# Kernel tuning notes

Measured on AMD Instinct MI355X. Metric: run time of the kernel, lower is better.

The kernel has to match this reference:

```python
import jax, jax.numpy as jnp
import numpy as np

B = 32768
T = 1024  # num_time_bins


def setup_inputs() -> dict:
    key = jax.random.key(0)
    k1, k2, k3, k4 = jax.random.split(key, 4)
    hazard_values = jax.random.uniform(k1, (B, T), dtype=jnp.float32)
    labels_Y = jax.random.uniform(k2, (B,), dtype=jnp.float32) * T
    # nn.Linear(T, T): weight [T, T] (out, in), bias [T]
    lim = 1.0 / np.sqrt(T)
    W = jax.random.uniform(k3, (T, T), minval=-lim, maxval=lim, dtype=jnp.float32)
    b = jax.random.uniform(k4, (T,), minval=-lim, maxval=lim, dtype=jnp.float32)
    return {"hazard_values": hazard_values, "labels_Y": labels_Y, "W": W, "b": b}


def reference(hazard_values, labels_Y, W, b):
    # linear + sigmoid + argmax -> per-row truncation position
    logits = hazard_values @ W.T + b                       # [B, T]
    trunc_pos = jnp.argmax(jax.nn.sigmoid(logits), axis=1, keepdims=True)  # [B, 1] int
    # survival curve
    S = jnp.cumprod(1.0 - hazard_values, axis=1)           # [B, T]
    # vectorized truncation decay: for t >= p, multiply by exp(-(t - p))
    t = jnp.arange(T)[None, :]                             # [1, T]
    decay = jnp.where(t >= trunc_pos,
                      jnp.exp(-(t - trunc_pos).astype(S.dtype)),
                      jnp.ones((), S.dtype))
    S = S * decay
    # MSE between argmax position and labels (original prints; we skip prints)
    p = trunc_pos[:, 0].astype(jnp.float32)
    truncation_loss = jnp.mean((p - labels_Y) ** 2)
    return trunc_pos, S, truncation_loss
```

## Files before the change

kernel.cpp:

```cpp
#include <hip/hip_runtime.h>

#define B_ROWS 32768
#define T_BINS 1024

typedef __attribute__((ext_vector_type(8))) _Float16 half8;
typedef __attribute__((ext_vector_type(4))) float floatx4;

__device__ __forceinline__ unsigned long long pack_max(float v, int col) {
    unsigned x = __float_as_uint(v);
    x = (x & 0x80000000u) ? ~x : (x | 0x80000000u);
    return ((unsigned long long)x << 32) | (unsigned)(~col);
}

__device__ __forceinline__ void async16h(const _Float16* g, _Float16* l) {
    __builtin_amdgcn_global_load_lds(
        (const __attribute__((address_space(1))) unsigned int*)g,
        (__attribute__((address_space(3))) unsigned int*)l,
        16, 0, 0);
}

__global__ __launch_bounds__(256) void tof16_kernel(
    const float* __restrict__ src, _Float16* __restrict__ dst, int n4)
{
    int idx = blockIdx.x * 256 + threadIdx.x;
    if (idx >= n4) return;
    float4 x = ((const float4*)src)[idx];
    union { _Float16 h[4]; ushort4 u; } cv;
    cv.h[0] = (_Float16)x.x;
    cv.h[1] = (_Float16)x.y;
    cv.h[2] = (_Float16)x.z;
    cv.h[3] = (_Float16)x.w;
    ((ushort4*)dst)[idx] = cv.u;
}

__global__ __launch_bounds__(256, 2) void mega_kernel(
    const float* __restrict__ A, const _Float16* __restrict__ Wh,
    const float* __restrict__ bias, const float* __restrict__ labels,
    float* __restrict__ out_trunc, float* __restrict__ out_S,
    float* __restrict__ loss_acc)
{
    __shared__ _Float16 sA[64 * 32];
    __shared__ _Float16 sW[256 * 32];
    __shared__ unsigned long long cand[4][64];
    __shared__ float trunc_s[64];

    const int tid  = threadIdx.x;
    const int lane = tid & 63;
    const int wc   = tid >> 6;
    const int by   = blockIdx.x;

    const int arow = tid >> 2;
    const int akg  = (tid & 3) * 8;
    const float* Abase = A + (size_t)(by * 64 + arow) * T_BINS + akg;
    _Float16* sAdst = &sA[arow * 32 + akg];

    const int ko = (lane >> 4) * 8;

    float run_best[4][4];
    int   run_col[4][4];
#pragma unroll
    for (int i = 0; i < 4; ++i)
#pragma unroll
        for (int r = 0; r < 4; ++r) { run_best[i][r] = -3.4e38f; run_col[i][r] = 0; }

    float4 pa0 = *(const float4*)(Abase);
    float4 pa1 = *(const float4*)(Abase + 4);

    for (int bx = 0; bx < 4; ++bx) {
        const int colbase = bx * 256 + wc * 64 + (lane & 15);
        float bj[4];
#pragma unroll
        for (int j = 0; j < 4; ++j) bj[j] = bias[colbase + j * 16];

        floatx4 acc[4][4];
#pragma unroll
        for (int i = 0; i < 4; ++i)
#pragma unroll
            for (int j = 0; j < 4; ++j) acc[i][j] = (floatx4){0.f, 0.f, 0.f, 0.f};

        for (int k0 = 0; k0 < T_BINS; k0 += 32) {
            half8 hv;
            hv[0] = (_Float16)pa0.x; hv[1] = (_Float16)pa0.y;
            hv[2] = (_Float16)pa0.z; hv[3] = (_Float16)pa0.w;
            hv[4] = (_Float16)pa1.x; hv[5] = (_Float16)pa1.y;
            hv[6] = (_Float16)pa1.z; hv[7] = (_Float16)pa1.w;
            *(half8*)sAdst = hv;
#pragma unroll
            for (int r = 0; r < 4; ++r) {
                int c = r * 256 + tid;
                int wrow = c >> 2, wkc = (c & 3) * 8;
                async16h(Wh + (size_t)(bx * 256 + wrow) * T_BINS + k0 + wkc,
                         &sW[(r * 256 + wc * 64) * 8]);
            }
            int kn = (k0 + 32) & (T_BINS - 1);
            pa0 = *(const float4*)(Abase + kn);
            pa1 = *(const float4*)(Abase + kn + 4);
            asm volatile("s_waitcnt vmcnt(0)" ::: "memory");
            __syncthreads();
            half8 ah[4], wh[4];
#pragma unroll
            for (int i = 0; i < 4; ++i)
                ah[i] = *(const half8*)&sA[(i * 16 + (lane & 15)) * 32 + ko];
#pragma unroll
            for (int j = 0; j < 4; ++j)
                wh[j] = *(const half8*)&sW[(wc * 64 + j * 16 + (lane & 15)) * 32 + ko];
#pragma unroll
            for (int i = 0; i < 4; ++i)
#pragma unroll
                for (int j = 0; j < 4; ++j)
                    acc[i][j] = __builtin_amdgcn_mfma_f32_16x16x32_f16(ah[i], wh[j], acc[i][j], 0, 0, 0);
            __syncthreads();
        }

#pragma unroll
        for (int i = 0; i < 4; ++i)
#pragma unroll
            for (int r = 0; r < 4; ++r)
#pragma unroll
                for (int j = 0; j < 4; ++j) {
                    float v = acc[i][j][r] + bj[j];
                    if (v > run_best[i][r]) { run_best[i][r] = v; run_col[i][r] = colbase + j * 16; }
                }
    }

#pragma unroll
    for (int i = 0; i < 4; ++i)
#pragma unroll
        for (int r = 0; r < 4; ++r) {
            float best = run_best[i][r];
            int   bc   = run_col[i][r];
#pragma unroll
            for (int off = 8; off >= 1; off >>= 1) {
                float ov = __shfl_xor(best, off, 64);
                int   oc = __shfl_xor(bc, off, 64);
                if (ov > best || (ov == best && oc < bc)) { best = ov; bc = oc; }
            }
            if ((lane & 15) == 0)
                cand[wc][i * 16 + (lane >> 4) * 4 + r] = pack_max(best, bc);
        }
    __syncthreads();

    if (tid < 64) {
        unsigned long long m01 = cand[0][tid] > cand[1][tid] ? cand[0][tid] : cand[1][tid];
        unsigned long long m23 = cand[2][tid] > cand[3][tid] ? cand[2][tid] : cand[3][tid];
        unsigned long long m = m01 > m23 ? m01 : m23;
        unsigned col = ~(unsigned)m;
        float p = (float)col;
        int rowG = by * 64 + tid;
        out_trunc[rowG] = p;
        trunc_s[tid] = p;
        float d = p - labels[rowG];
        float term = d * d * (1.0f / (float)B_ROWS);
#pragma unroll
        for (int off = 32; off >= 1; off >>= 1)
            term += __shfl_down(term, off, 64);
        if (tid == 0) atomicAdd(loss_acc, term);
    }
    __syncthreads();

    for (int rr = 0; rr < 16; ++rr) {
        int row  = wc * 16 + rr;
        int rowG = by * 64 + row;
        const float* Hrow = A + (size_t)rowG * T_BINS + lane * 16;
        float4 h0 = *(const float4*)(Hrow + 0);
        float4 h1 = *(const float4*)(Hrow + 4);
        float4 h2 = *(const float4*)(Hrow + 8);
        float4 h3 = *(const float4*)(Hrow + 12);
        float hv[16] = {h0.x, h0.y, h0.z, h0.w, h1.x, h1.y, h1.z, h1.w,
                        h2.x, h2.y, h2.z, h2.w, h3.x, h3.y, h3.z, h3.w};
        float vprod[16];
        float run = 1.f;
#pragma unroll
        for (int j = 0; j < 16; ++j) { run *= (1.f - hv[j]); vprod[j] = run; }
        float x = run;
#pragma unroll
        for (int off = 1; off < 64; off <<= 1) {
            float o = __shfl_up(x, off, 64);
            if (lane >= off) x *= o;
        }
        float pre = __shfl_up(x, 1, 64);
        if (lane == 0) pre = 1.f;

        int p  = (int)trunc_s[row];
        int t0 = lane * 16;
        float sv[16];
#pragma unroll
        for (int j = 0; j < 16; ++j) {
            float s = pre * vprod[j];
            int t = t0 + j;
            if (t >= p) s *= __expf((float)(p - t));
            sv[j] = s;
        }
        float* Srow = out_S + (size_t)rowG * T_BINS + lane * 16;
        *(float4*)(Srow + 0)  = (float4){sv[0],  sv[1],  sv[2],  sv[3]};
        *(float4*)(Srow + 4)  = (float4){sv[4],  sv[5],  sv[6],  sv[7]};
        *(float4*)(Srow + 8)  = (float4){sv[8],  sv[9],  sv[10], sv[11]};
        *(float4*)(Srow + 12) = (float4){sv[12], sv[13], sv[14], sv[15]};
    }
}

#define BMf 64
#define BKf 16
#define LDSS (BMf + 4)
__global__ __launch_bounds__(256) void gemm_argmax_fp32(
    const float* __restrict__ A, const float* __restrict__ W,
    const float* __restrict__ bias, unsigned long long* __restrict__ rec)
{
    __shared__ float As[BKf][LDSS];
    __shared__ float Ws[BKf][LDSS];
    const int tid = threadIdx.x;
    const int tx = tid & 15, ty = tid >> 4;
    const int bx = blockIdx.x, by = blockIdx.y;
    const int ar = tid >> 2, ak = (tid & 3) << 2;
    const float* Arow = A + (size_t)(by * BMf + ar) * T_BINS + ak;
    const float* Wrow = W + (size_t)(bx * BMf + ar) * T_BINS + ak;
    float acc[4][4];
#pragma unroll
    for (int i = 0; i < 4; ++i)
#pragma unroll
        for (int j = 0; j < 4; ++j) acc[i][j] = 0.f;
    for (int k0 = 0; k0 < T_BINS; k0 += BKf) {
        float4 av = *(const float4*)(Arow + k0);
        float4 wvv = *(const float4*)(Wrow + k0);
        As[ak + 0][ar] = av.x; As[ak + 1][ar] = av.y; As[ak + 2][ar] = av.z; As[ak + 3][ar] = av.w;
        Ws[ak + 0][ar] = wvv.x; Ws[ak + 1][ar] = wvv.y; Ws[ak + 2][ar] = wvv.z; Ws[ak + 3][ar] = wvv.w;
        __syncthreads();
#pragma unroll
        for (int k = 0; k < BKf; ++k) {
            float4 a4 = *(const float4*)&As[k][ty * 4];
            float4 w4 = *(const float4*)&Ws[k][tx * 4];
            float aa[4] = {a4.x, a4.y, a4.z, a4.w};
            float ww[4] = {w4.x, w4.y, w4.z, w4.w};
#pragma unroll
            for (int i = 0; i < 4; ++i)
#pragma unroll
                for (int j = 0; j < 4; ++j) acc[i][j] = fmaf(aa[i], ww[j], acc[i][j]);
        }
        __syncthreads();
    }
    const int colBase = bx * BMf + tx * 4;
    float bv[4];
#pragma unroll
    for (int j = 0; j < 4; ++j) bv[j] = bias[colBase + j];
#pragma unroll
    for (int i = 0; i < 4; ++i) {
        float best = acc[i][0] + bv[0];
        int bc = colBase;
#pragma unroll
        for (int j = 1; j < 4; ++j) {
            float v = acc[i][j] + bv[j];
            if (v > best) { best = v; bc = colBase + j; }
        }
#pragma unroll
        for (int off = 8; off >= 1; off >>= 1) {
            float ov = __shfl_xor(best, off, 64);
            int oc = __shfl_xor(bc, off, 64);
            if (ov > best || (ov == best && oc < bc)) { best = ov; bc = oc; }
        }
        if (tx == 0) atomicMax(&rec[by * BMf + ty * 4 + i], pack_max(best, bc));
    }
}

__global__ __launch_bounds__(256) void finalize_kernel(
    const unsigned long long* __restrict__ rec, const float* __restrict__ labels,
    float* __restrict__ out_trunc, float* __restrict__ loss_acc)
{
    int i = blockIdx.x * 256 + threadIdx.x;
    unsigned col = ~(unsigned)(rec[i] & 0xFFFFFFFFull);
    float p = (float)col;
    out_trunc[i] = p;
    float d = p - labels[i];
    float term = d * d * (1.0f / (float)B_ROWS);
#pragma unroll
    for (int off = 32; off >= 1; off >>= 1)
        term += __shfl_down(term, off, 64);
    __shared__ float partials[4];
    int lane = threadIdx.x & 63, wv = threadIdx.x >> 6;
    if (lane == 0) partials[wv] = term;
    __syncthreads();
    if (threadIdx.x == 0)
        atomicAdd(loss_acc, partials[0] + partials[1] + partials[2] + partials[3]);
}

__global__ __launch_bounds__(256) void scan_kernel_f32(
    const float* __restrict__ H, const float* __restrict__ trunc_f,
    float* __restrict__ Sout)
{
    const int row = blockIdx.x;
    const int tid = threadIdx.x;
    const int lane = tid & 63;
    const int wv = tid >> 6;
    const float4 h = *(const float4*)(H + (size_t)row * T_BINS + tid * 4);
    float l0 = 1.f - h.x;
    float l1 = l0 * (1.f - h.y);
    float l2 = l1 * (1.f - h.z);
    float l3 = l2 * (1.f - h.w);
    float x = l3;
#pragma unroll
    for (int off = 1; off < 64; off <<= 1) {
        float o = __shfl_up(x, off, 64);
        if (lane >= off) x *= o;
    }
    float ex = __shfl_up(x, 1, 64);
    if (lane == 0) ex = 1.f;
    __shared__ float wtot[4];
    if (lane == 63) wtot[wv] = x;
    __syncthreads();
    float wpre = 1.f;
#pragma unroll
    for (int w = 0; w < 3; ++w)
        if (w < wv) wpre *= wtot[w];
    float pre = wpre * ex;
    int p = (int)trunc_f[row];
    int t0 = tid * 4;
    float sv[4] = {pre * l0, pre * l1, pre * l2, pre * l3};
#pragma unroll
    for (int j = 0; j < 4; ++j) {
        int t = t0 + j;
        if (t >= p) sv[j] *= __expf((float)(p - t));
    }
    float4 s4 = {sv[0], sv[1], sv[2], sv[3]};
    *(float4*)(Sout + (size_t)row * T_BINS + tid * 4) = s4;
}

extern "C" void kernel_launch(void* const* d_in, const int* in_sizes, int n_in,
                              void* d_out, int out_size, void* d_ws, size_t ws_size,
                              hipStream_t stream)
{
    const float* hazard = (const float*)d_in[0];
    const float* labels = (const float*)d_in[1];
    const float* W      = (const float*)d_in[2];
    const float* bias   = (const float*)d_in[3];

    float* out       = (float*)d_out;
    float* out_trunc = out;
    float* out_S     = out + B_ROWS;
    float* out_loss  = out + B_ROWS + (size_t)B_ROWS * T_BINS;

    hipMemsetAsync(out_loss, 0, sizeof(float), stream);

    const size_t NW = (size_t)T_BINS * T_BINS;
    if (ws_size >= NW * sizeof(_Float16)) {
        _Float16* Wh = (_Float16*)d_ws;
        tof16_kernel<<<(int)(NW / 4 / 256), 256, 0, stream>>>(W, Wh, (int)(NW / 4));
        mega_kernel<<<B_ROWS / 64, 256, 0, stream>>>(
            hazard, Wh, bias, labels, out_trunc, out_S, out_loss);
    } else {
        unsigned long long* rec = (unsigned long long*)out_S;
        hipMemsetAsync(rec, 0, (size_t)B_ROWS * sizeof(unsigned long long), stream);
        dim3 ggrid(T_BINS / BMf, B_ROWS / BMf);
        gemm_argmax_fp32<<<ggrid, 256, 0, stream>>>(hazard, W, bias, rec);
        finalize_kernel<<<B_ROWS / 256, 256, 0, stream>>>(rec, labels, out_trunc, out_loss);
        scan_kernel_f32<<<B_ROWS, 256, 0, stream>>>(hazard, out_trunc, out_S);
    }
}
```

Measured before the change: 379.5 us.

## Double-buffer LDS tiles to overlap global loads with MFMA compute

Splits the A and W shared-memory tiles into two buffers. The next k-step's W tile is prefetched asynchronously into the alternate buffer and the A tile is staged there as well, while MFMAs run on the current buffer. The old full vmcnt(0) wait and the two barriers per step become a partial wait and a single barrier, and all bias values are loaded once up front. This hides global-load latency behind compute, at the cost of doubled LDS usage, which may lower occupancy, and more intricate wait-count correctness.

```diff
diff --git a/kernel.cpp b/kernel.cpp
--- a/kernel.cpp
+++ b/kernel.cpp
@@ -39,8 +39,8 @@
     float* __restrict__ out_trunc, float* __restrict__ out_S,
     float* __restrict__ loss_acc)
 {
-    __shared__ _Float16 sA[64 * 32];
-    __shared__ _Float16 sW[256 * 32];
+    __shared__ _Float16 sA[2][64 * 32];
+    __shared__ _Float16 sW[2][256 * 32];
     __shared__ unsigned long long cand[4][64];
     __shared__ float trunc_s[64];
 
@@ -52,9 +52,16 @@
     const int arow = tid >> 2;
     const int akg  = (tid & 3) * 8;
     const float* Abase = A + (size_t)(by * 64 + arow) * T_BINS + akg;
-    _Float16* sAdst = &sA[arow * 32 + akg];
+    const int sAoff = arow * 32 + akg;
 
     const int ko = (lane >> 4) * 8;
+
+    float bj_all[4][4];
+#pragma unroll
+    for (int bx = 0; bx < 4; ++bx)
+#pragma unroll
+        for (int j = 0; j < 4; ++j)
+            bj_all[bx][j] = bias[bx * 256 + wc * 64 + (lane & 15) + j * 16];
 
     float run_best[4][4];
     int   run_col[4][4];
@@ -63,62 +70,89 @@
 #pragma unroll
         for (int r = 0; r < 4; ++r) { run_best[i][r] = -3.4e38f; run_col[i][r] = 0; }
 
-    float4 pa0 = *(const float4*)(Abase);
-    float4 pa1 = *(const float4*)(Abase + 4);
-
+    {
+        float4 f0 = *(const float4*)(Abase);
+        float4 f1 = *(const float4*)(Abase + 4);
+        half8 hv;
+        hv[0] = (_Float16)f0.x; hv[1] = (_Float16)f0.y;
+        hv[2] = (_Float16)f0.z; hv[3] = (_Float16)f0.w;
+        hv[4] = (_Float16)f1.x; hv[5] = (_Float16)f1.y;
+        hv[6] = (_Float16)f1.z; hv[7] = (_Float16)f1.w;
+        *(half8*)&sA[0][sAoff] = hv;
+    }
+#pragma unroll
+    for (int r = 0; r < 4; ++r) {
+        int c = r * 256 + tid;
+        int wrow = c >> 2, wkc = (c & 3) * 8;
+        async16h(Wh + (size_t)wrow * T_BINS + wkc, &sW[0][(r * 256 + wc * 64) * 8]);
+    }
+    asm volatile("" ::: "memory");
+    float4 pa0 = *(const float4*)(Abase + 32);
+    float4 pa1 = *(const float4*)(Abase + 36);
+    asm volatile("s_waitcnt vmcnt(2) lgkmcnt(0)" ::: "memory");
+    __builtin_amdgcn_s_barrier();
+
+    int n = 0;
     for (int bx = 0; bx < 4; ++bx) {
-        const int colbase = bx * 256 + wc * 64 + (lane & 15);
-        float bj[4];
-#pragma unroll
-        for (int j = 0; j < 4; ++j) bj[j] = bias[colbase + j * 16];
-
         floatx4 acc[4][4];
 #pragma unroll
         for (int i = 0; i < 4; ++i)
 #pragma unroll
             for (int j = 0; j < 4; ++j) acc[i][j] = (floatx4){0.f, 0.f, 0.f, 0.f};
 
-        for (int k0 = 0; k0 < T_BINS; k0 += 32) {
-            half8 hv;
-            hv[0] = (_Float16)pa0.x; hv[1] = (_Float16)pa0.y;
-            hv[2] = (_Float16)pa0.z; hv[3] = (_Float16)pa0.w;
-            hv[4] = (_Float16)pa1.x; hv[5] = (_Float16)pa1.y;
-            hv[6] = (_Float16)pa1.z; hv[7] = (_Float16)pa1.w;
-            *(half8*)sAdst = hv;
+        for (int t = 0; t < 32; ++t, ++n) {
+            const int cur = n & 1;
+            const int m   = (n + 1) & 127;
+            const int bxn = m >> 5;
+            const int k0n = (m & 31) * 32;
+
 #pragma unroll
             for (int r = 0; r < 4; ++r) {
                 int c = r * 256 + tid;
                 int wrow = c >> 2, wkc = (c & 3) * 8;
-                async16h(Wh + (size_t)(bx * 256 + wrow) * T_BINS + k0 + wkc,
-                         &sW[(r * 256 + wc * 64) * 8]);
+                async16h(Wh + (size_t)(bxn * 256 + wrow) * T_BINS + k0n + wkc,
+                         &sW[cur ^ 1][(r * 256 + wc * 64) * 8]);
             }
-            int kn = (k0 + 32) & (T_BINS - 1);
-            pa0 = *(const float4*)(Abase + kn);
-            pa1 = *(const float4*)(Abase + kn + 4);
-            asm volatile("s_waitcnt vmcnt(0)" ::: "memory");
-            __syncthreads();
-            half8 ah[4], wh[4];
+            asm volatile("" ::: "memory");
+            {
+                half8 hv;
+                hv[0] = (_Float16)pa0.x; hv[1] = (_Float16)pa0.y;
+                hv[2] = (_Float16)pa0.z; hv[3] = (_Float16)pa0.w;
+                hv[4] = (_Float16)pa1.x; hv[5] = (_Float16)pa1.y;
+                hv[6] = (_Float16)pa1.z; hv[7] = (_Float16)pa1.w;
+                *(half8*)&sA[cur ^ 1][sAoff] = hv;
+            }
+            asm volatile("" ::: "memory");
+            {
+                int kq = ((n + 2) & 31) * 32;
+                pa0 = *(const float4*)(Abase + kq);
+                pa1 = *(const float4*)(Abase + kq + 4);
+            }
+            asm volatile("" ::: "memory");
+            half8 ah[4], whf[4];
 #pragma unroll
             for (int i = 0; i < 4; ++i)
-                ah[i] = *(const half8*)&sA[(i * 16 + (lane & 15)) * 32 + ko];
+                ah[i] = *(const half8*)&sA[cur][(i * 16 + (lane & 15)) * 32 + ko];
 #pragma unroll
             for (int j = 0; j < 4; ++j)
-                wh[j] = *(const half8*)&sW[(wc * 64 + j * 16 + (lane & 15)) * 32 + ko];
+                whf[j] = *(const half8*)&sW[cur][(wc * 64 + j * 16 + (lane & 15)) * 32 + ko];
 #pragma unroll
             for (int i = 0; i < 4; ++i)
 #pragma unroll
                 for (int j = 0; j < 4; ++j)
-                    acc[i][j] = __builtin_amdgcn_mfma_f32_16x16x32_f16(ah[i], wh[j], acc[i][j], 0, 0, 0);
-            __syncthreads();
-        }
-
+                    acc[i][j] = __builtin_amdgcn_mfma_f32_16x16x32_f16(ah[i], whf[j], acc[i][j], 0, 0, 0);
+            asm volatile("s_waitcnt vmcnt(2) lgkmcnt(0)" ::: "memory");
+            __builtin_amdgcn_s_barrier();
+        }
+
+        const int colbase = bx * 256 + wc * 64 + (lane & 15);
 #pragma unroll
         for (int i = 0; i < 4; ++i)
 #pragma unroll
             for (int r = 0; r < 4; ++r)
 #pragma unroll
                 for (int j = 0; j < 4; ++j) {
-                    float v = acc[i][j][r] + bj[j];
+                    float v = acc[i][j][r] + bj_all[bx][j];
                     if (v > run_best[i][r]) { run_best[i][r] = v; run_col[i][r] = colbase + j * 16; }
                 }
     }
@@ -143,8 +177,8 @@
     if (tid < 64) {
         unsigned long long m01 = cand[0][tid] > cand[1][tid] ? cand[0][tid] : cand[1][tid];
         unsigned long long m23 = cand[2][tid] > cand[3][tid] ? cand[2][tid] : cand[3][tid];
-        unsigned long long m = m01 > m23 ? m01 : m23;
-        unsigned col = ~(unsigned)m;
+        unsigned long long mm = m01 > m23 ? m01 : m23;
+        unsigned col = ~(unsigned)mm;
         float p = (float)col;
         int rowG = by * 64 + tid;
         out_trunc[rowG] = p;
```

New measurement: 400.4 us. 1.05x slower.
